# Kernel optimization log

Hardware: AMD Instinct MI355X
Metric: run time of the kernel (lower is better)

Reference implementation:

```python
import jax, jax.numpy as jnp
import numpy as np

DIM = 96
NUM_HEADS = 3
WIN = 7  # window_size (square)


def _relative_position_index(wh, ww):
    coords = np.stack(np.meshgrid(np.arange(wh), np.arange(ww), indexing='ij'))  # [2, wh, ww]
    flat = coords.reshape(2, -1)  # [2, n]
    rel = flat[:, :, None] - flat[:, None, :]  # [2, n, n]
    rel = rel.transpose(1, 2, 0).astype(np.int64)
    rel[..., 0] += wh - 1
    rel[..., 1] += ww - 1
    rel[..., 0] *= 2 * ww - 1
    return rel.sum(-1)  # [n, n]


def setup_inputs() -> dict:
    key = jax.random.key(0)
    ks = jax.random.split(key, 9)
    b, n, c = 8192, WIN * WIN, DIM
    std = 0.02
    inp = {
        'x': jax.random.normal(ks[0], (b, n, c), jnp.float32),
        'v': jax.random.normal(ks[1], (b, n, c), jnp.float32),
        'w_q': jax.random.normal(ks[2], (c, c), jnp.float32) * std,
        'b_q': jnp.zeros((c,), jnp.float32),
        'w_kv': jax.random.normal(ks[3], (c, 2 * c), jnp.float32) * std,
        'b_kv': jnp.zeros((2 * c,), jnp.float32),
        'w_proj': jax.random.normal(ks[4], (c, c), jnp.float32) * std,
        'b_proj': jnp.zeros((c,), jnp.float32),
        'rpb_table': jax.random.normal(ks[5], ((2 * WIN - 1) * (2 * WIN - 1), NUM_HEADS), jnp.float32) * std,
        'rel_index': jnp.asarray(_relative_position_index(WIN, WIN), jnp.int32),
    }
    return inp


def reference(x, v, w_q, b_q, w_kv, b_kv, w_proj, b_proj, rpb_table, rel_index):
    b, n, c = x.shape
    h = NUM_HEADS
    hd = c // h
    scale = hd ** -0.5
    # q: [b, h, n, hd]
    q = (x @ w_q + b_q).reshape(b, n, h, hd).transpose(0, 2, 1, 3) * scale
    kv = (v @ w_kv + b_kv).reshape(b, n, 2, h, hd)
    k = kv[:, :, 0].transpose(0, 2, 1, 3)  # [b, h, n, hd]
    vv = kv[:, :, 1].transpose(0, 2, 1, 3)
    attn = jnp.einsum('bhqd,bhkd->bhqk', q, k)  # [b, h, n, n]
    bias = rpb_table[rel_index.reshape(-1)].reshape(n, n, h).transpose(2, 0, 1)  # [h, n, n]
    attn = jax.nn.softmax(attn + bias[None], axis=-1)
    out = jnp.einsum('bhqk,bhkd->bhqd', attn, vv).transpose(0, 2, 1, 3).reshape(b, n, c)
    return out @ w_proj + b_proj
```

## Files before the change

kernel.cpp:

```cpp
#include <hip/hip_runtime.h>
#include <hip/hip_bf16.h>

typedef __bf16 bf16x8 __attribute__((ext_vector_type(8)));
typedef float f32x4 __attribute__((ext_vector_type(4)));
typedef short s16x8 __attribute__((ext_vector_type(8)));
typedef short s16x4 __attribute__((ext_vector_type(4)));

#define NTOK 49
#define CDIM 96
#define KS_S 104
#define VT_S 56
#define BN_S 136
#define LOG2E 1.4426950408889634f

#if __has_builtin(__builtin_amdgcn_exp2f)
#define EXP2F(x) __builtin_amdgcn_exp2f(x)
#else
#define EXP2F(x) exp2f(x)
#endif

#define DRAIN() do { asm volatile("s_waitcnt lgkmcnt(0)" ::: "memory"); \
                     __builtin_amdgcn_sched_barrier(0); } while (0)

__device__ __forceinline__ unsigned short f2bf(float f) {
  __hip_bfloat16 h = __float2bfloat16(f);
  return __builtin_bit_cast(unsigned short, h);
}

__device__ __forceinline__ unsigned int cvtpk(float lo, float hi) {
  unsigned int r;
  asm("v_cvt_pk_bf16_f32 %0, %1, %2" : "=v"(r) : "v"(lo), "v"(hi));
  return r;
}
__device__ __forceinline__ unsigned short f2bf_f(float f) {
  return (unsigned short)cvtpk(f, f);
}
__device__ __forceinline__ s16x4 pack4(float a, float b, float c, float d) {
  union { unsigned int u[2]; s16x4 v; } r;
  r.u[0] = cvtpk(a, b); r.u[1] = cvtpk(c, d);
  return r.v;
}

__device__ __forceinline__ bf16x8 ld_cvt8(const float* p) {
  float4 a = *(const float4*)p;
  float4 b = *(const float4*)(p + 4);
  union { unsigned int u[4]; bf16x8 v; } r;
  r.u[0] = cvtpk(a.x, a.y); r.u[1] = cvtpk(a.z, a.w);
  r.u[2] = cvtpk(b.x, b.y); r.u[3] = cvtpk(b.z, b.w);
  return r.v;
}

__global__ void prep(const float* __restrict__ wq, const float* __restrict__ wkv,
                     const float* __restrict__ wproj, const float* __restrict__ rpb,
                     const int* __restrict__ relidx, unsigned short* __restrict__ wsT,
                     float* __restrict__ biasf) {
  const int total = 36864 + 3 * 49 * 64;
  for (int i = blockIdx.x * 256 + threadIdx.x; i < total; i += gridDim.x * 256) {
    if (i < 9216) {
      int oc = i / 96, ic = i - oc * 96;
      wsT[i] = f2bf(wq[ic * 96 + oc]);
    } else if (i < 27648) {
      int j = i - 9216; int oc = j / 96, ic = j - oc * 96;
      wsT[i] = f2bf(wkv[ic * 192 + oc]);
    } else if (i < 36864) {
      int j = i - 27648; int oc = j / 96, ic = j - oc * 96;
      wsT[i] = f2bf(wproj[ic * 96 + oc]);
    } else {
      int j = i - 36864; int h = j / 3136; int rc = j - h * 3136;
      int r = rc >> 6, c = rc & 63;
      biasf[j] = (c < 49) ? rpb[relidx[r * 49 + c] * 3 + h] * LOG2E : 0.f;
    }
  }
}

__launch_bounds__(256, 3)
__global__ void attn_fused(const float* __restrict__ xg, const float* __restrict__ vg,
                           const float* __restrict__ bq, const float* __restrict__ bkv,
                           const float* __restrict__ bproj,
                           const unsigned short* __restrict__ wsT,
                           const float* __restrict__ biasf,
                           float* __restrict__ outg) {
  __shared__ __align__(16) unsigned char smem[38352];
  unsigned short* Ks  = (unsigned short*)smem;
  unsigned short* VVT = (unsigned short*)(smem + 10192);

  const int tid = threadIdx.x, lane = tid & 63, wv = tid >> 6;
  const int c16 = lane & 15, g4 = lane >> 4;
  const int win = blockIdx.x;
  const int q0 = (wv == 0) ? 0 : (wv == 1) ? 16 : (wv == 2) ? 32 : 33;
  unsigned short* bnc = (unsigned short*)(smem + 20944) + wv * (16 * BN_S);

  const int mp = wv & 1;
  const bool isK = (wv < 2);
  const int m0 = mp ? 32 : 0;
  const int m1 = mp ? 33 : 16;

  const float* base = xg + (size_t)win * (NTOK * CDIM);
  const float* vbase = vg + (size_t)win * (NTOK * CDIM);
  const float* xrow = base + (q0 + c16) * CDIM;
  const float* vrow0 = vbase + (m0 + c16) * CDIM;
  const float* vrow1 = vbase + (m1 + c16) * CDIM;

  bf16x8 xf[3], vf0[3], vf1[3];
#pragma unroll
  for (int k = 0; k < 3; ++k) {
    xf[k]  = ld_cvt8(xrow  + k * 32 + g4 * 8);
    vf0[k] = ld_cvt8(vrow0 + k * 32 + g4 * 8);
    vf1[k] = ld_cvt8(vrow1 + k * 32 + g4 * 8);
  }

  float bqv[6], bkvv[6];
#pragma unroll
  for (int nt = 0; nt < 6; ++nt) {
    bqv[nt]  = bq[nt * 16 + c16];
    bkvv[nt] = bkv[(isK ? 0 : 96) + nt * 16 + c16];
  }

  const float scale = 0.2550348742f;
  const unsigned short* wkvBase = wsT + 9216 + (isK ? 0 : 9216);

  {
    bf16x8 wqf[2][3], wkf[2][3];
#pragma unroll
    for (int k = 0; k < 3; ++k) {
      wqf[0][k] = *(const bf16x8*)(wsT     + c16 * 96 + k * 32 + g4 * 8);
      wkf[0][k] = *(const bf16x8*)(wkvBase + c16 * 96 + k * 32 + g4 * 8);
    }
#pragma unroll
    for (int nt = 0; nt < 6; ++nt) {
      const int cur = nt & 1, nxt = cur ^ 1;
      if (nt < 5) {
#pragma unroll
        for (int k = 0; k < 3; ++k) {
          wqf[nxt][k] = *(const bf16x8*)(wsT     + ((nt + 1) * 16 + c16) * 96 + k * 32 + g4 * 8);
          wkf[nxt][k] = *(const bf16x8*)(wkvBase + ((nt + 1) * 16 + c16) * 96 + k * 32 + g4 * 8);
        }
      }
      f32x4 aq = {0,0,0,0}, a0 = {0,0,0,0}, a1 = {0,0,0,0};
      __builtin_amdgcn_s_setprio(1);
#pragma unroll
      for (int k = 0; k < 3; ++k) {
        aq = __builtin_amdgcn_mfma_f32_16x16x32_bf16(xf[k],  wqf[cur][k], aq, 0, 0, 0);
        a0 = __builtin_amdgcn_mfma_f32_16x16x32_bf16(vf0[k], wkf[cur][k], a0, 0, 0, 0);
        a1 = __builtin_amdgcn_mfma_f32_16x16x32_bf16(vf1[k], wkf[cur][k], a1, 0, 0, 0);
      }
      __builtin_amdgcn_s_setprio(0);
      {
        const int ocl = nt * 16 + c16;
        float bias = bqv[nt];
#pragma unroll
        for (int r = 0; r < 4; ++r)
          bnc[(4 * g4 + r) * BN_S + ocl] = f2bf_f((aq[r] + bias) * scale);
      }
      {
        float bias = bkvv[nt];
        if (isK) {
          const int ocl = nt * 16 + c16;
#pragma unroll
          for (int r = 0; r < 4; ++r)
            Ks[(m0 + 4 * g4 + r) * KS_S + ocl] = f2bf_f(a0[r] + bias);
#pragma unroll
          for (int r = 0; r < 4; ++r)
            Ks[(m1 + 4 * g4 + r) * KS_S + ocl] = f2bf_f(a1[r] + bias);
        } else {
          const int dim = nt * 16 + c16;
          *(s16x4*)(VVT + dim * VT_S + (m0 + 4 * g4)) =
              pack4(a0[0] + bias, a0[1] + bias, a0[2] + bias, a0[3] + bias);
          if (mp == 0) {
            *(s16x4*)(VVT + dim * VT_S + (16 + 4 * g4)) =
                pack4(a1[0] + bias, a1[1] + bias, a1[2] + bias, a1[3] + bias);
          } else {
#pragma unroll
            for (int r = 0; r < 4; ++r)
              VVT[dim * VT_S + 33 + 4 * g4 + r] = f2bf_f(a1[r] + bias);
          }
        }
      }
    }
  }
  __syncthreads();

  const int q = q0 + c16;
  s16x8 vmask;
#pragma unroll
  for (int j = 0; j < 8; ++j)
    vmask[j] = (short)(((32 + g4 * 8 + j) < 49) ? 0xFFFF : 0x0000);

  f32x4 oacc[6] = {{0,0,0,0},{0,0,0,0},{0,0,0,0},{0,0,0,0},{0,0,0,0},{0,0,0,0}};

  auto softmax_pw = [&](const f32x4* s, const f32x4* bv, int pcol) {
    float vals[16];
#pragma unroll
    for (int kt = 0; kt < 4; ++kt)
#pragma unroll
      for (int r = 0; r < 4; ++r) {
        int key = 16 * kt + 4 * g4 + r;
        vals[kt * 4 + r] = (kt < 3 || key < 49) ? (s[kt][r] + bv[kt][r]) : -1e30f;
      }
    float m8[8];
#pragma unroll
    for (int j = 0; j < 8; ++j) m8[j] = fmaxf(vals[j], vals[j + 8]);
    float ma = fmaxf(m8[0], m8[4]), mb = fmaxf(m8[1], m8[5]);
    float mc = fmaxf(m8[2], m8[6]), md = fmaxf(m8[3], m8[7]);
    float mx = fmaxf(fmaxf(ma, mb), fmaxf(mc, md));
    mx = fmaxf(mx, __shfl_xor(mx, 16, 64));
    mx = fmaxf(mx, __shfl_xor(mx, 32, 64));
    float e[16];
#pragma unroll
    for (int j = 0; j < 16; ++j) e[j] = EXP2F(vals[j] - mx);
    float s8[8];
#pragma unroll
    for (int j = 0; j < 8; ++j) s8[j] = e[j] + e[j + 8];
    float sa = s8[0] + s8[4], sb = s8[1] + s8[5], sc = s8[2] + s8[6], sd = s8[3] + s8[7];
    float sum = (sa + sb) + (sc + sd);
    sum += __shfl_xor(sum, 16, 64);
    sum += __shfl_xor(sum, 32, 64);
    float rinv = 1.0f / sum;
#pragma unroll
    for (int kt = 0; kt < 4; ++kt)
      *(s16x4*)(bnc + c16 * BN_S + pcol + 16 * kt + 4 * g4) =
          pack4(e[kt*4] * rinv, e[kt*4+1] * rinv, e[kt*4+2] * rinv, e[kt*4+3] * rinv);
  };

  auto pv_out = [&](int h, int pcol, int ocol) {
    bf16x8 ap0 = *(const bf16x8*)(bnc + c16 * BN_S + pcol + g4 * 8);
    bf16x8 ap1 = *(const bf16x8*)(bnc + c16 * BN_S + pcol + 32 + g4 * 8);
    bf16x8 bva[2]; s16x8 bvb[2];
#pragma unroll
    for (int dt = 0; dt < 2; ++dt) {
      int dim = h * 32 + dt * 16 + c16;
      bva[dt] = *(const bf16x8*)(VVT + dim * VT_S + g4 * 8);
      s16x8 t = *(const s16x8*)(VVT + dim * VT_S + 32 + g4 * 8);
      bvb[dt] = t & vmask;
    }
    f32x4 o[2];
    __builtin_amdgcn_s_setprio(1);
#pragma unroll
    for (int dt = 0; dt < 2; ++dt) {
      o[dt] = __builtin_amdgcn_mfma_f32_16x16x32_bf16(ap0, bva[dt], (f32x4){0,0,0,0}, 0, 0, 0);
      o[dt] = __builtin_amdgcn_mfma_f32_16x16x32_bf16(ap1, __builtin_bit_cast(bf16x8, bvb[dt]), o[dt], 0, 0, 0);
    }
    __builtin_amdgcn_s_setprio(0);
#pragma unroll
    for (int dt = 0; dt < 2; ++dt)
#pragma unroll
      for (int r = 0; r < 4; ++r)
        bnc[(4 * g4 + r) * BN_S + ocol + dt * 16 + c16] = f2bf_f(o[dt][r]);
  };

  auto oproj = [&](int h, int ocol) {
    bf16x8 bo = *(const bf16x8*)(bnc + c16 * BN_S + ocol + g4 * 8);
    bf16x8 wa[6];
#pragma unroll
    for (int mt = 0; mt < 6; ++mt)
      wa[mt] = *(const bf16x8*)(wsT + 27648 + (mt * 16 + c16) * 96 + h * 32 + g4 * 8);
    __builtin_amdgcn_s_setprio(1);
#pragma unroll
    for (int mt = 0; mt < 6; ++mt)
      oacc[mt] = __builtin_amdgcn_mfma_f32_16x16x32_bf16(wa[mt], bo, oacc[mt], 0, 0, 0);
    __builtin_amdgcn_s_setprio(0);
  };

  f32x4 b0v[4], b1v[4];
  {
    const float* br0 = biasf + q * 64 + 4 * g4;
    const float* br1 = biasf + (49 + q) * 64 + 4 * g4;
#pragma unroll
    for (int kt = 0; kt < 4; ++kt) {
      b0v[kt] = *(const f32x4*)(br0 + 16 * kt);
      b1v[kt] = *(const f32x4*)(br1 + 16 * kt);
    }
  }
  bf16x8 qf0 = *(const bf16x8*)(bnc + c16 * BN_S + g4 * 8);
  bf16x8 qf1 = *(const bf16x8*)(bnc + c16 * BN_S + 32 + g4 * 8);
  bf16x8 qf2 = *(const bf16x8*)(bnc + c16 * BN_S + 64 + g4 * 8);

  f32x4 s0[4], s1[4];
  {
    bf16x8 ak0[4], ak1[4];
#pragma unroll
    for (int kt = 0; kt < 4; ++kt) {
      ak0[kt] = *(const bf16x8*)(Ks + (16 * kt + c16) * KS_S + g4 * 8);
      ak1[kt] = *(const bf16x8*)(Ks + (16 * kt + c16) * KS_S + 32 + g4 * 8);
    }
    __builtin_amdgcn_s_setprio(1);
#pragma unroll
    for (int kt = 0; kt < 4; ++kt)
      s0[kt] = __builtin_amdgcn_mfma_f32_16x16x32_bf16(ak0[kt], qf0, (f32x4){0,0,0,0}, 0, 0, 0);
#pragma unroll
    for (int kt = 0; kt < 4; ++kt)
      s1[kt] = __builtin_amdgcn_mfma_f32_16x16x32_bf16(ak1[kt], qf1, (f32x4){0,0,0,0}, 0, 0, 0);
    __builtin_amdgcn_s_setprio(0);
  }
  softmax_pw(s0, b0v, 0);
  softmax_pw(s1, b1v, 64);

  f32x4 b2v[4];
  {
    const float* br2 = biasf + (98 + q) * 64 + 4 * g4;
#pragma unroll
    for (int kt = 0; kt < 4; ++kt) b2v[kt] = *(const f32x4*)(br2 + 16 * kt);
  }
  f32x4 s2[4];
  {
    bf16x8 ak2[4];
#pragma unroll
    for (int kt = 0; kt < 4; ++kt)
      ak2[kt] = *(const bf16x8*)(Ks + (16 * kt + c16) * KS_S + 64 + g4 * 8);
    __builtin_amdgcn_s_setprio(1);
#pragma unroll
    for (int kt = 0; kt < 4; ++kt)
      s2[kt] = __builtin_amdgcn_mfma_f32_16x16x32_bf16(ak2[kt], qf2, (f32x4){0,0,0,0}, 0, 0, 0);
    __builtin_amdgcn_s_setprio(0);
  }

  DRAIN();
  pv_out(0, 0, 0);
  pv_out(1, 64, 32);
  softmax_pw(s2, b2v, 64);

  DRAIN();
  oproj(0, 0);
  oproj(1, 32);
  pv_out(2, 64, 96);

  DRAIN();
  oproj(2, 96);

  {
    const bool store_ok = (wv < 3) || (c16 == 15);
    float* orow = outg + (size_t)win * (NTOK * CDIM) + q * 96;
#pragma unroll
    for (int mt = 0; mt < 6; ++mt) {
      int oc0 = mt * 16 + g4 * 4;
      if (store_ok) {
        float4 bb = *(const float4*)(bproj + oc0);
        float4 o4;
        o4.x = oacc[mt][0] + bb.x; o4.y = oacc[mt][1] + bb.y;
        o4.z = oacc[mt][2] + bb.z; o4.w = oacc[mt][3] + bb.w;
        *(float4*)(orow + oc0) = o4;
      }
    }
  }
}

extern "C" void kernel_launch(void* const* d_in, const int* in_sizes, int n_in,
                              void* d_out, int out_size, void* d_ws, size_t ws_size,
                              hipStream_t stream) {
  const float* x     = (const float*)d_in[0];
  const float* v     = (const float*)d_in[1];
  const float* wq    = (const float*)d_in[2];
  const float* bq    = (const float*)d_in[3];
  const float* wkv   = (const float*)d_in[4];
  const float* bkv   = (const float*)d_in[5];
  const float* wproj = (const float*)d_in[6];
  const float* bproj = (const float*)d_in[7];
  const float* rpb   = (const float*)d_in[8];
  const int*   relidx= (const int*)d_in[9];
  float* out = (float*)d_out;
  unsigned short* wsT = (unsigned short*)d_ws;
  float* biasf = (float*)((char*)d_ws + 73728);
  int nwin = in_sizes[0] / (NTOK * CDIM);

  hipLaunchKernelGGL(prep, dim3(181), dim3(256), 0, stream,
                     wq, wkv, wproj, rpb, relidx, wsT, biasf);
  hipLaunchKernelGGL(attn_fused, dim3(nwin), dim3(256), 0, stream,
                     x, v, bq, bkv, bproj, wsT, biasf, out);
}
```

Before: 253.9 us.

## Fold value and output projections into per-head combined weights

Precomputes per-head products W_v[:,h] @ W_proj[h,:] in the prep kernel, plus a folded output bias, so the fused kernel projects v straight into per-head projected values and accumulates attn @ VP directly into the output. This removes the separate PV-then-oproj stages and their shared-memory round trips. The cost is a larger value projection (18 tiles instead of 6) and roughly double the LDS footprint, so launch bounds drop to two blocks per CU. Each wave now computes its own K/Q rows, and all three heads' softmax runs before a single PV-projection pass. Folding the weights before bf16 rounding also changes the numerics slightly.

```diff
diff --git a/kernel.cpp b/kernel.cpp
--- a/kernel.cpp
+++ b/kernel.cpp
@@ -10,7 +10,7 @@
 #define CDIM 96
 #define KS_S 104
 #define VT_S 56
-#define BN_S 136
+#define BN_S 192
 #define LOG2E 1.4426950408889634f
 
 #if __has_builtin(__builtin_amdgcn_exp2f)
@@ -26,7 +26,6 @@
   __hip_bfloat16 h = __float2bfloat16(f);
   return __builtin_bit_cast(unsigned short, h);
 }
-
 __device__ __forceinline__ unsigned int cvtpk(float lo, float hi) {
   unsigned int r;
   asm("v_cvt_pk_bf16_f32 %0, %1, %2" : "=v"(r) : "v"(lo), "v"(hi));
@@ -40,7 +39,6 @@
   r.u[0] = cvtpk(a, b); r.u[1] = cvtpk(c, d);
   return r.v;
 }
-
 __device__ __forceinline__ bf16x8 ld_cvt8(const float* p) {
   float4 a = *(const float4*)p;
   float4 b = *(const float4*)(p + 4);
@@ -52,130 +50,134 @@
 
 __global__ void prep(const float* __restrict__ wq, const float* __restrict__ wkv,
                      const float* __restrict__ wproj, const float* __restrict__ rpb,
-                     const int* __restrict__ relidx, unsigned short* __restrict__ wsT,
-                     float* __restrict__ biasf) {
-  const int total = 36864 + 3 * 49 * 64;
+                     const int* __restrict__ relidx, const float* __restrict__ bkv,
+                     const float* __restrict__ bproj,
+                     unsigned short* __restrict__ wsT, float* __restrict__ biasf,
+                     float* __restrict__ btot) {
+  const int total = 46080 + 3 * 49 * 64 + 96;
   for (int i = blockIdx.x * 256 + threadIdx.x; i < total; i += gridDim.x * 256) {
     if (i < 9216) {
       int oc = i / 96, ic = i - oc * 96;
       wsT[i] = f2bf(wq[ic * 96 + oc]);
-    } else if (i < 27648) {
+    } else if (i < 18432) {
       int j = i - 9216; int oc = j / 96, ic = j - oc * 96;
       wsT[i] = f2bf(wkv[ic * 192 + oc]);
-    } else if (i < 36864) {
-      int j = i - 27648; int oc = j / 96, ic = j - oc * 96;
-      wsT[i] = f2bf(wproj[ic * 96 + oc]);
-    } else {
-      int j = i - 36864; int h = j / 3136; int rc = j - h * 3136;
+    } else if (i < 46080) {
+      int j = i - 18432; int h = j / 9216; int rem = j - h * 9216;
+      int oc = rem / 96, ic = rem - oc * 96;
+      float s = 0.f;
+      for (int d = 0; d < 32; ++d)
+        s += wkv[ic * 192 + 96 + h * 32 + d] * wproj[(h * 32 + d) * 96 + oc];
+      wsT[i] = f2bf(s);
+    } else if (i < 46080 + 9408) {
+      int j = i - 46080; int h = j / 3136; int rc = j - h * 3136;
       int r = rc >> 6, c = rc & 63;
       biasf[j] = (c < 49) ? rpb[relidx[r * 49 + c] * 3 + h] * LOG2E : 0.f;
-    }
-  }
-}
-
-__launch_bounds__(256, 3)
+    } else {
+      int oc = i - (46080 + 9408);
+      float s = bproj[oc];
+      for (int j = 0; j < 96; ++j) s += bkv[96 + j] * wproj[j * 96 + oc];
+      btot[oc] = s;
+    }
+  }
+}
+
+__launch_bounds__(256, 2)
 __global__ void attn_fused(const float* __restrict__ xg, const float* __restrict__ vg,
                            const float* __restrict__ bq, const float* __restrict__ bkv,
-                           const float* __restrict__ bproj,
                            const unsigned short* __restrict__ wsT,
                            const float* __restrict__ biasf,
+                           const float* __restrict__ btot,
                            float* __restrict__ outg) {
-  __shared__ __align__(16) unsigned char smem[38352];
+  __shared__ __align__(16) unsigned char smem[67024];
   unsigned short* Ks  = (unsigned short*)smem;
-  unsigned short* VVT = (unsigned short*)(smem + 10192);
+  unsigned short* VPT = (unsigned short*)(smem + 10192);
 
   const int tid = threadIdx.x, lane = tid & 63, wv = tid >> 6;
   const int c16 = lane & 15, g4 = lane >> 4;
   const int win = blockIdx.x;
   const int q0 = (wv == 0) ? 0 : (wv == 1) ? 16 : (wv == 2) ? 32 : 33;
-  unsigned short* bnc = (unsigned short*)(smem + 20944) + wv * (16 * BN_S);
-
-  const int mp = wv & 1;
-  const bool isK = (wv < 2);
-  const int m0 = mp ? 32 : 0;
-  const int m1 = mp ? 33 : 16;
-
-  const float* base = xg + (size_t)win * (NTOK * CDIM);
-  const float* vbase = vg + (size_t)win * (NTOK * CDIM);
-  const float* xrow = base + (q0 + c16) * CDIM;
-  const float* vrow0 = vbase + (m0 + c16) * CDIM;
-  const float* vrow1 = vbase + (m1 + c16) * CDIM;
-
-  bf16x8 xf[3], vf0[3], vf1[3];
+  unsigned short* bnc = (unsigned short*)(smem + 42448) + wv * (16 * BN_S);
+
+  const float* xrow = xg + (size_t)win * (NTOK * CDIM) + (q0 + c16) * CDIM;
+  const float* vrow = vg + (size_t)win * (NTOK * CDIM) + (q0 + c16) * CDIM;
+
+  bf16x8 xf[3], vf[3];
 #pragma unroll
   for (int k = 0; k < 3; ++k) {
-    xf[k]  = ld_cvt8(xrow  + k * 32 + g4 * 8);
-    vf0[k] = ld_cvt8(vrow0 + k * 32 + g4 * 8);
-    vf1[k] = ld_cvt8(vrow1 + k * 32 + g4 * 8);
-  }
-
+    xf[k] = ld_cvt8(xrow + k * 32 + g4 * 8);
+    vf[k] = ld_cvt8(vrow + k * 32 + g4 * 8);
+  }
   float bqv[6], bkvv[6];
 #pragma unroll
   for (int nt = 0; nt < 6; ++nt) {
     bqv[nt]  = bq[nt * 16 + c16];
-    bkvv[nt] = bkv[(isK ? 0 : 96) + nt * 16 + c16];
-  }
-
-  const float scale = 0.2550348742f;
-  const unsigned short* wkvBase = wsT + 9216 + (isK ? 0 : 9216);
+    bkvv[nt] = bkv[nt * 16 + c16];
+  }
+
+#pragma unroll
+  for (int pass = 0; pass < 2; ++pass) {
+    f32x4 acc[9] = {{0,0,0,0},{0,0,0,0},{0,0,0,0},{0,0,0,0},{0,0,0,0},
+                    {0,0,0,0},{0,0,0,0},{0,0,0,0},{0,0,0,0}};
+#pragma unroll
+    for (int kf = 0; kf < 3; ++kf) {
+      bf16x8 wf[9];
+#pragma unroll
+      for (int u9 = 0; u9 < 9; ++u9) {
+        int u = pass * 9 + u9;
+        int h = u / 6, oct = u - h * 6;
+        wf[u9] = *(const bf16x8*)(wsT + 18432 + h * 9216 +
+                                  (oct * 16 + c16) * 96 + kf * 32 + g4 * 8);
+      }
+      __builtin_amdgcn_s_setprio(1);
+#pragma unroll
+      for (int u9 = 0; u9 < 9; ++u9)
+        acc[u9] = __builtin_amdgcn_mfma_f32_16x16x32_bf16(vf[kf], wf[u9], acc[u9], 0, 0, 0);
+      __builtin_amdgcn_s_setprio(0);
+    }
+#pragma unroll
+    for (int u9 = 0; u9 < 9; ++u9) {
+      int u = pass * 9 + u9;
+      int h = u / 6, oct = u - h * 6;
+      unsigned short* row = VPT + (h * 96 + oct * 16 + c16) * VT_S;
+      if (wv < 3) {
+        *(s16x4*)(row + q0 + 4 * g4) = pack4(acc[u9][0], acc[u9][1], acc[u9][2], acc[u9][3]);
+      } else {
+#pragma unroll
+        for (int r = 0; r < 4; ++r) row[q0 + 4 * g4 + r] = f2bf_f(acc[u9][r]);
+      }
+    }
+  }
 
   {
-    bf16x8 wqf[2][3], wkf[2][3];
-#pragma unroll
-    for (int k = 0; k < 3; ++k) {
-      wqf[0][k] = *(const bf16x8*)(wsT     + c16 * 96 + k * 32 + g4 * 8);
-      wkf[0][k] = *(const bf16x8*)(wkvBase + c16 * 96 + k * 32 + g4 * 8);
-    }
-#pragma unroll
-    for (int nt = 0; nt < 6; ++nt) {
-      const int cur = nt & 1, nxt = cur ^ 1;
-      if (nt < 5) {
-#pragma unroll
-        for (int k = 0; k < 3; ++k) {
-          wqf[nxt][k] = *(const bf16x8*)(wsT     + ((nt + 1) * 16 + c16) * 96 + k * 32 + g4 * 8);
-          wkf[nxt][k] = *(const bf16x8*)(wkvBase + ((nt + 1) * 16 + c16) * 96 + k * 32 + g4 * 8);
-        }
-      }
-      f32x4 aq = {0,0,0,0}, a0 = {0,0,0,0}, a1 = {0,0,0,0};
+    f32x4 kacc[6] = {{0,0,0,0},{0,0,0,0},{0,0,0,0},{0,0,0,0},{0,0,0,0},{0,0,0,0}};
+    f32x4 qacc[6] = {{0,0,0,0},{0,0,0,0},{0,0,0,0},{0,0,0,0},{0,0,0,0},{0,0,0,0}};
+#pragma unroll
+    for (int kf = 0; kf < 3; ++kf) {
+      bf16x8 wkf[6], wqf[6];
+#pragma unroll
+      for (int oct = 0; oct < 6; ++oct) {
+        wkf[oct] = *(const bf16x8*)(wsT + 9216 + (oct * 16 + c16) * 96 + kf * 32 + g4 * 8);
+        wqf[oct] = *(const bf16x8*)(wsT +        (oct * 16 + c16) * 96 + kf * 32 + g4 * 8);
+      }
       __builtin_amdgcn_s_setprio(1);
 #pragma unroll
-      for (int k = 0; k < 3; ++k) {
-        aq = __builtin_amdgcn_mfma_f32_16x16x32_bf16(xf[k],  wqf[cur][k], aq, 0, 0, 0);
-        a0 = __builtin_amdgcn_mfma_f32_16x16x32_bf16(vf0[k], wkf[cur][k], a0, 0, 0, 0);
-        a1 = __builtin_amdgcn_mfma_f32_16x16x32_bf16(vf1[k], wkf[cur][k], a1, 0, 0, 0);
+      for (int oct = 0; oct < 6; ++oct) {
+        kacc[oct] = __builtin_amdgcn_mfma_f32_16x16x32_bf16(vf[kf], wkf[oct], kacc[oct], 0, 0, 0);
+        qacc[oct] = __builtin_amdgcn_mfma_f32_16x16x32_bf16(xf[kf], wqf[oct], qacc[oct], 0, 0, 0);
       }
       __builtin_amdgcn_s_setprio(0);
-      {
-        const int ocl = nt * 16 + c16;
-        float bias = bqv[nt];
-#pragma unroll
-        for (int r = 0; r < 4; ++r)
-          bnc[(4 * g4 + r) * BN_S + ocl] = f2bf_f((aq[r] + bias) * scale);
-      }
-      {
-        float bias = bkvv[nt];
-        if (isK) {
-          const int ocl = nt * 16 + c16;
-#pragma unroll
-          for (int r = 0; r < 4; ++r)
-            Ks[(m0 + 4 * g4 + r) * KS_S + ocl] = f2bf_f(a0[r] + bias);
-#pragma unroll
-          for (int r = 0; r < 4; ++r)
-            Ks[(m1 + 4 * g4 + r) * KS_S + ocl] = f2bf_f(a1[r] + bias);
-        } else {
-          const int dim = nt * 16 + c16;
-          *(s16x4*)(VVT + dim * VT_S + (m0 + 4 * g4)) =
-              pack4(a0[0] + bias, a0[1] + bias, a0[2] + bias, a0[3] + bias);
-          if (mp == 0) {
-            *(s16x4*)(VVT + dim * VT_S + (16 + 4 * g4)) =
-                pack4(a1[0] + bias, a1[1] + bias, a1[2] + bias, a1[3] + bias);
-          } else {
-#pragma unroll
-            for (int r = 0; r < 4; ++r)
-              VVT[dim * VT_S + 33 + 4 * g4 + r] = f2bf_f(a1[r] + bias);
-          }
-        }
-      }
+    }
+    const float scale = 0.2550348742f;
+#pragma unroll
+    for (int oct = 0; oct < 6; ++oct) {
+      float kb = bkvv[oct], qb = bqv[oct];
+#pragma unroll
+      for (int r = 0; r < 4; ++r)
+        Ks[(q0 + 4 * g4 + r) * KS_S + oct * 16 + c16] = f2bf_f(kacc[oct][r] + kb);
+#pragma unroll
+      for (int r = 0; r < 4; ++r)
+        bnc[(4 * g4 + r) * BN_S + oct * 16 + c16] = f2bf_f((qacc[oct][r] + qb) * scale);
     }
   }
   __syncthreads();
@@ -186,7 +188,25 @@
   for (int j = 0; j < 8; ++j)
     vmask[j] = (short)(((32 + g4 * 8 + j) < 49) ? 0xFFFF : 0x0000);
 
-  f32x4 oacc[6] = {{0,0,0,0},{0,0,0,0},{0,0,0,0},{0,0,0,0},{0,0,0,0},{0,0,0,0}};
+  f32x4 b0v[4], b1v[4], b2v[4];
+  {
+    const float* br0 = biasf + q * 64 + 4 * g4;
+    const float* br1 = biasf + (49 + q) * 64 + 4 * g4;
+    const float* br2 = biasf + (98 + q) * 64 + 4 * g4;
+#pragma unroll
+    for (int kt = 0; kt < 4; ++kt) {
+      b0v[kt] = *(const f32x4*)(br0 + 16 * kt);
+      b1v[kt] = *(const f32x4*)(br1 + 16 * kt);
+      b2v[kt] = *(const f32x4*)(br2 + 16 * kt);
+    }
+  }
+  float btotv[6];
+#pragma unroll
+  for (int oct = 0; oct < 6; ++oct) btotv[oct] = btot[oct * 16 + c16];
+
+  bf16x8 qf0 = *(const bf16x8*)(bnc + c16 * BN_S + g4 * 8);
+  bf16x8 qf1 = *(const bf16x8*)(bnc + c16 * BN_S + 32 + g4 * 8);
+  bf16x8 qf2 = *(const bf16x8*)(bnc + c16 * BN_S + 64 + g4 * 8);
 
   auto softmax_pw = [&](const f32x4* s, const f32x4* bv, int pcol) {
     float vals[16];
@@ -222,123 +242,61 @@
           pack4(e[kt*4] * rinv, e[kt*4+1] * rinv, e[kt*4+2] * rinv, e[kt*4+3] * rinv);
   };
 
-  auto pv_out = [&](int h, int pcol, int ocol) {
-    bf16x8 ap0 = *(const bf16x8*)(bnc + c16 * BN_S + pcol + g4 * 8);
-    bf16x8 ap1 = *(const bf16x8*)(bnc + c16 * BN_S + pcol + 32 + g4 * 8);
-    bf16x8 bva[2]; s16x8 bvb[2];
-#pragma unroll
-    for (int dt = 0; dt < 2; ++dt) {
-      int dim = h * 32 + dt * 16 + c16;
-      bva[dt] = *(const bf16x8*)(VVT + dim * VT_S + g4 * 8);
-      s16x8 t = *(const s16x8*)(VVT + dim * VT_S + 32 + g4 * 8);
-      bvb[dt] = t & vmask;
-    }
-    f32x4 o[2];
-    __builtin_amdgcn_s_setprio(1);
-#pragma unroll
-    for (int dt = 0; dt < 2; ++dt) {
-      o[dt] = __builtin_amdgcn_mfma_f32_16x16x32_bf16(ap0, bva[dt], (f32x4){0,0,0,0}, 0, 0, 0);
-      o[dt] = __builtin_amdgcn_mfma_f32_16x16x32_bf16(ap1, __builtin_bit_cast(bf16x8, bvb[dt]), o[dt], 0, 0, 0);
-    }
-    __builtin_amdgcn_s_setprio(0);
-#pragma unroll
-    for (int dt = 0; dt < 2; ++dt)
-#pragma unroll
-      for (int r = 0; r < 4; ++r)
-        bnc[(4 * g4 + r) * BN_S + ocol + dt * 16 + c16] = f2bf_f(o[dt][r]);
-  };
-
-  auto oproj = [&](int h, int ocol) {
-    bf16x8 bo = *(const bf16x8*)(bnc + c16 * BN_S + ocol + g4 * 8);
-    bf16x8 wa[6];
-#pragma unroll
-    for (int mt = 0; mt < 6; ++mt)
-      wa[mt] = *(const bf16x8*)(wsT + 27648 + (mt * 16 + c16) * 96 + h * 32 + g4 * 8);
-    __builtin_amdgcn_s_setprio(1);
-#pragma unroll
-    for (int mt = 0; mt < 6; ++mt)
-      oacc[mt] = __builtin_amdgcn_mfma_f32_16x16x32_bf16(wa[mt], bo, oacc[mt], 0, 0, 0);
-    __builtin_amdgcn_s_setprio(0);
-  };
-
-  f32x4 b0v[4], b1v[4];
+  f32x4 s0[4], s1[4], s2[4];
   {
-    const float* br0 = biasf + q * 64 + 4 * g4;
-    const float* br1 = biasf + (49 + q) * 64 + 4 * g4;
-#pragma unroll
-    for (int kt = 0; kt < 4; ++kt) {
-      b0v[kt] = *(const f32x4*)(br0 + 16 * kt);
-      b1v[kt] = *(const f32x4*)(br1 + 16 * kt);
-    }
-  }
-  bf16x8 qf0 = *(const bf16x8*)(bnc + c16 * BN_S + g4 * 8);
-  bf16x8 qf1 = *(const bf16x8*)(bnc + c16 * BN_S + 32 + g4 * 8);
-  bf16x8 qf2 = *(const bf16x8*)(bnc + c16 * BN_S + 64 + g4 * 8);
-
-  f32x4 s0[4], s1[4];
-  {
-    bf16x8 ak0[4], ak1[4];
+    bf16x8 ak0[4], ak1[4], ak2[4];
 #pragma unroll
     for (int kt = 0; kt < 4; ++kt) {
       ak0[kt] = *(const bf16x8*)(Ks + (16 * kt + c16) * KS_S + g4 * 8);
       ak1[kt] = *(const bf16x8*)(Ks + (16 * kt + c16) * KS_S + 32 + g4 * 8);
+      ak2[kt] = *(const bf16x8*)(Ks + (16 * kt + c16) * KS_S + 64 + g4 * 8);
     }
     __builtin_amdgcn_s_setprio(1);
 #pragma unroll
-    for (int kt = 0; kt < 4; ++kt)
+    for (int kt = 0; kt < 4; ++kt) {
       s0[kt] = __builtin_amdgcn_mfma_f32_16x16x32_bf16(ak0[kt], qf0, (f32x4){0,0,0,0}, 0, 0, 0);
-#pragma unroll
-    for (int kt = 0; kt < 4; ++kt)
       s1[kt] = __builtin_amdgcn_mfma_f32_16x16x32_bf16(ak1[kt], qf1, (f32x4){0,0,0,0}, 0, 0, 0);
+      s2[kt] = __builtin_amdgcn_mfma_f32_16x16x32_bf16(ak2[kt], qf2, (f32x4){0,0,0,0}, 0, 0, 0);
+    }
     __builtin_amdgcn_s_setprio(0);
   }
+
   softmax_pw(s0, b0v, 0);
   softmax_pw(s1, b1v, 64);
-
-  f32x4 b2v[4];
+  softmax_pw(s2, b2v, 128);
+  DRAIN();
+
+  bf16x8 ap[3][2];
+#pragma unroll
+  for (int h = 0; h < 3; ++h) {
+    ap[h][0] = *(const bf16x8*)(bnc + c16 * BN_S + h * 64 + g4 * 8);
+    ap[h][1] = *(const bf16x8*)(bnc + c16 * BN_S + h * 64 + 32 + g4 * 8);
+  }
+  f32x4 facc[6] = {{0,0,0,0},{0,0,0,0},{0,0,0,0},{0,0,0,0},{0,0,0,0},{0,0,0,0}};
+#pragma unroll
+  for (int h = 0; h < 3; ++h) {
+#pragma unroll
+    for (int oct = 0; oct < 6; ++oct) {
+      const unsigned short* row = VPT + (h * 96 + oct * 16 + c16) * VT_S;
+      bf16x8 bv0 = *(const bf16x8*)(row + g4 * 8);
+      s16x8 t = *(const s16x8*)(row + 32 + g4 * 8);
+      t &= vmask;
+      facc[oct] = __builtin_amdgcn_mfma_f32_16x16x32_bf16(ap[h][0], bv0, facc[oct], 0, 0, 0);
+      facc[oct] = __builtin_amdgcn_mfma_f32_16x16x32_bf16(ap[h][1], __builtin_bit_cast(bf16x8, t), facc[oct], 0, 0, 0);
+    }
+  }
+
   {
-    const float* br2 = biasf + (98 + q) * 64 + 4 * g4;
-#pragma unroll
-    for (int kt = 0; kt < 4; ++kt) b2v[kt] = *(const f32x4*)(br2 + 16 * kt);
-  }
-  f32x4 s2[4];
-  {
-    bf16x8 ak2[4];
-#pragma unroll
-    for (int kt = 0; kt < 4; ++kt)
-      ak2[kt] = *(const bf16x8*)(Ks + (16 * kt + c16) * KS_S + 64 + g4 * 8);
-    __builtin_amdgcn_s_setprio(1);
-#pragma unroll
-    for (int kt = 0; kt < 4; ++kt)
-      s2[kt] = __builtin_amdgcn_mfma_f32_16x16x32_bf16(ak2[kt], qf2, (f32x4){0,0,0,0}, 0, 0, 0);
-    __builtin_amdgcn_s_setprio(0);
-  }
-
-  DRAIN();
-  pv_out(0, 0, 0);
-  pv_out(1, 64, 32);
-  softmax_pw(s2, b2v, 64);
-
-  DRAIN();
-  oproj(0, 0);
-  oproj(1, 32);
-  pv_out(2, 64, 96);
-
-  DRAIN();
-  oproj(2, 96);
-
-  {
-    const bool store_ok = (wv < 3) || (c16 == 15);
-    float* orow = outg + (size_t)win * (NTOK * CDIM) + q * 96;
-#pragma unroll
-    for (int mt = 0; mt < 6; ++mt) {
-      int oc0 = mt * 16 + g4 * 4;
-      if (store_ok) {
-        float4 bb = *(const float4*)(bproj + oc0);
-        float4 o4;
-        o4.x = oacc[mt][0] + bb.x; o4.y = oacc[mt][1] + bb.y;
-        o4.z = oacc[mt][2] + bb.z; o4.w = oacc[mt][3] + bb.w;
-        *(float4*)(orow + oc0) = o4;
+    float* obase = outg + (size_t)win * (NTOK * CDIM);
+#pragma unroll
+    for (int oct = 0; oct < 6; ++oct) {
+      float bt = btotv[oct];
+#pragma unroll
+      for (int r = 0; r < 4; ++r) {
+        if (wv < 3 || (4 * g4 + r) == 15) {
+          int tok = q0 + 4 * g4 + r;
+          obase[tok * 96 + oct * 16 + c16] = facc[oct][r] + bt;
+        }
       }
     }
   }
@@ -359,11 +317,12 @@
   const int*   relidx= (const int*)d_in[9];
   float* out = (float*)d_out;
   unsigned short* wsT = (unsigned short*)d_ws;
-  float* biasf = (float*)((char*)d_ws + 73728);
+  float* biasf = (float*)((char*)d_ws + 92160);
+  float* btot  = (float*)((char*)d_ws + 129792);
   int nwin = in_sizes[0] / (NTOK * CDIM);
 
-  hipLaunchKernelGGL(prep, dim3(181), dim3(256), 0, stream,
-                     wq, wkv, wproj, rpb, relidx, wsT, biasf);
+  hipLaunchKernelGGL(prep, dim3(218), dim3(256), 0, stream,
+                     wq, wkv, wproj, rpb, relidx, bkv, bproj, wsT, biasf, btot);
   hipLaunchKernelGGL(attn_fused, dim3(nwin), dim3(256), 0, stream,
-                     x, v, bq, bkv, bproj, wsT, biasf, out);
-}
+                     x, v, bq, bkv, wsT, biasf, btot, out);
+}
```

New measurement: 313.1 us. 23.3% more time.
